# Performance work log

Measured on AMD Instinct MI355X. Metric: run time of the kernel, lower is better.

Reference implementation:

```python
import math
import jax, jax.numpy as jnp
import numpy as np

V, D, H, L, F, S, B = 32000, 768, 12, 6, 3072, 2048, 4
DK = D // H


def setup_inputs() -> dict:
    key = jax.random.key(0)
    ks = jax.random.split(key, 16)
    sc = 0.02
    n = jax.random.normal
    inp = {
        "input_ids": jax.random.randint(ks[0], (B, S), 0, V, dtype=jnp.int64)
        if jax.config.jax_enable_x64 else jax.random.randint(ks[0], (B, S), 0, V, dtype=jnp.int32),
        "emb": n(ks[1], (V, D), jnp.float32) * sc,
        "Wq": n(ks[2], (L, D, D), jnp.float32) * sc, "bq": jnp.zeros((L, D), jnp.float32),
        "Wk": n(ks[3], (L, D, D), jnp.float32) * sc, "bk": jnp.zeros((L, D), jnp.float32),
        "Wv": n(ks[4], (L, D, D), jnp.float32) * sc, "bv": jnp.zeros((L, D), jnp.float32),
        "Wo": n(ks[5], (L, D, D), jnp.float32) * sc, "bo": jnp.zeros((L, D), jnp.float32),
        "W1": n(ks[6], (L, D, F), jnp.float32) * sc, "b1": jnp.zeros((L, F), jnp.float32),
        "W2": n(ks[7], (L, F, D), jnp.float32) * sc, "b2": jnp.zeros((L, D), jnp.float32),
        "gamma": jnp.ones((L, D), jnp.float32), "beta": jnp.zeros((L, D), jnp.float32),
    }
    return inp


def _pos_encoding(seq_len, d):
    pos = jnp.arange(seq_len, dtype=jnp.float32)[:, None]                  # [S,1]
    div = jnp.exp(jnp.arange(0, d, 2, dtype=jnp.float32) * (-math.log(10000.0) / d))
    ang = pos * div                                                        # [S,D/2]
    return jnp.stack([jnp.sin(ang), jnp.cos(ang)], axis=-1).reshape(seq_len, d)


def _layernorm(x, g, b, eps=1e-5):
    mu = x.mean(-1, keepdims=True)
    var = ((x - mu) ** 2).mean(-1, keepdims=True)
    return (x - mu) * jax.lax.rsqrt(var + eps) * g + b


def _forward(input_ids, emb, Wq, bq, Wk, bk, Wv, bv, Wo, bo, W1, b1, W2, b2, gamma, beta):
    mask = (input_ids != 1)[:, None, None, :]                              # [B,1,1,S]
    x = emb[input_ids] + _pos_encoding(input_ids.shape[1], emb.shape[1])   # [B,S,D]

    def layer(x, p):
        wq, bq_, wk, bk_, wv, bv_, wo, bo_, w1, b1_, w2, b2_, g, bt = p
        def heads(h):  # [B,S,D] -> [B,H,S,DK]
            return h.reshape(B, S, H, DK).transpose(0, 2, 1, 3)
        q = heads(x @ wq + bq_)
        k = heads(x @ wk + bk_)
        v = heads(x @ wv + bv_)
        scores = jnp.einsum("bhqd,bhkd->bhqk", q, k) / math.sqrt(DK)
        scores = jnp.where(mask, scores, -1e9)
        attn = jax.nn.softmax(scores, axis=-1)
        o = jnp.einsum("bhqk,bhkd->bhqd", attn, v)
        o = o.transpose(0, 2, 1, 3).reshape(B, S, D) @ wo + bo_
        x1 = _layernorm(x + o, g, bt)
        ff = jax.nn.relu(x1 @ w1 + b1_) @ w2 + b2_
        return _layernorm(x1 + ff, g, bt), None  # same norm params reused (as in source)

    x, _ = jax.lax.scan(layer, x, (Wq, bq, Wk, bk, Wv, bv, Wo, bo, W1, b1, W2, b2, gamma, beta))
    return x.mean(axis=1)                                                  # [B,D]


def reference(input_ids, emb, Wq, bq, Wk, bk, Wv, bv, Wo, bo, W1, b1, W2, b2, gamma, beta):
    return _forward(input_ids, emb, Wq, bq, Wk, bk, Wv, bv, Wo, bo, W1, b1, W2, b2, gamma, beta)
```

## Files before the change

kernel.cpp:

```cpp
#include <hip/hip_runtime.h>
#include <hip/hip_bf16.h>
#include <math.h>

typedef unsigned short u16;
typedef unsigned long long u64;
using bf16x8 = __attribute__((ext_vector_type(8))) short;
using f32x4  = __attribute__((ext_vector_type(4))) float;

static constexpr int kD = 768;
static constexpr int kH = 12;
static constexpr int kL = 6;
static constexpr int kF = 3072;
static constexpr int kS = 2048;
static constexpr int kB = 4;
static constexpr int kQW = 2304;
static constexpr int kNT = kB * kS;

static constexpr float kQScale = 0.18033688011112043f;

__device__ __forceinline__ u16 f2bf(float f) {
    return __bfloat16_as_ushort(__float2bfloat16(f));
}
__device__ __forceinline__ float b2f(u16 u) {
    return __uint_as_float((unsigned)u << 16);
}
__device__ __forceinline__ unsigned cvtpk(float a, float b) {
    unsigned d;
    asm volatile("v_cvt_pk_bf16_f32 %0, %1, %2" : "=v"(d) : "v"(a), "v"(b));
    return d;
}
__device__ __forceinline__ float exp2fast(float x) {
#if __has_builtin(__builtin_amdgcn_exp2f)
    return __builtin_amdgcn_exp2f(x);
#else
    return __expf(x * 0.6931471805599453f);
#endif
}

__device__ __forceinline__ void gload16(const void* g, void* l) {
    auto gp = reinterpret_cast<const __attribute__((address_space(1))) unsigned int*>(
        reinterpret_cast<uintptr_t>(g));
    auto lp = reinterpret_cast<__attribute__((address_space(3))) unsigned int*>(
        reinterpret_cast<uintptr_t>(l));
    __builtin_amdgcn_global_load_lds(gp, lp, 16, 0, 0);
}

__global__ __launch_bounds__(256) void embed_pe(
    const int* __restrict__ ids, const float* __restrict__ emb,
    u16* __restrict__ xbf)
{
    const int t = blockIdx.x;
    const int s = t & (kS - 1);
    const int id = ids[t];
#pragma unroll
    for (int j = 0; j < 3; ++j) {
        const int d = threadIdx.x + (j << 8);
        const float i2 = (float)((d >> 1) << 1);
        const float dv = __expf(i2 * (-9.210340371976184f / 768.f));
        const float ang = (float)s * dv;
        const float pe = (d & 1) ? cosf(ang) : sinf(ang);
        xbf[(size_t)t * kD + d] = f2bf(emb[(size_t)id * kD + d] + pe);
    }
}

__global__ __launch_bounds__(256) void embed_pe_f32(
    const int* __restrict__ ids, const float* __restrict__ emb,
    float* __restrict__ x)
{
    const int t = blockIdx.x;
    const int s = t & (kS - 1);
    const int id = ids[t];
#pragma unroll
    for (int j = 0; j < 3; ++j) {
        const int d = threadIdx.x + (j << 8);
        const float i2 = (float)((d >> 1) << 1);
        const float dv = __expf(i2 * (-9.210340371976184f / 768.f));
        const float ang = (float)s * dv;
        const float pe = (d & 1) ? cosf(ang) : sinf(ang);
        x[(size_t)t * kD + d] = emb[(size_t)id * kD + d] + pe;
    }
}

__global__ __launch_bounds__(64) void mk_maskbits(const int* __restrict__ ids,
                                                  u64* __restrict__ mbits)
{
    const int w = blockIdx.x;
    const int lane = threadIdx.x;
    const u64 m = __ballot(ids[(size_t)w * 64 + lane] != 1);
    if (lane == 0) mbits[w] = m;
}

__global__ __launch_bounds__(256) void bias_build(
    const float* __restrict__ bq, const float* __restrict__ bk,
    const float* __restrict__ bv, const float* __restrict__ bo,
    const float* __restrict__ b1, const float* __restrict__ b2,
    float* __restrict__ ba)
{
    const int i = blockIdx.x * 256 + threadIdx.x;
    if (i >= 6 * 6912) return;
    const int l = i / 6912, p = i % 6912;
    float v;
    if      (p < 768)  v = bq[l * 768 + p] * kQScale;
    else if (p < 1536) v = bk[l * 768 + p - 768];
    else if (p < 2304) v = bv[l * 768 + p - 1536];
    else if (p < 3072) v = bo[l * 768 + p - 2304];
    else if (p < 6144) v = b1[(size_t)l * 3072 + p - 3072];
    else               v = b2[l * 768 + p - 6144];
    ba[i] = v;
}

static constexpr size_t OFF_WO = (size_t)2304 * 768;
static constexpr size_t OFF_W1 = OFF_WO + (size_t)768 * 768;
static constexpr size_t OFF_W2 = OFF_W1 + (size_t)3072 * 768;
static constexpr size_t WARENA_E = OFF_W2 + (size_t)768 * 3072;

__global__ __launch_bounds__(256) void cvt_all(
    const float* __restrict__ Wq, const float* __restrict__ Wk,
    const float* __restrict__ Wv, const float* __restrict__ Wo,
    const float* __restrict__ W1, const float* __restrict__ W2,
    u16* __restrict__ wa)
{
    __shared__ float T[64][68];
    const int t = blockIdx.x;
    const float* S; u16* Dp; int Nsrc, Kdst, srow0, scol0; float sc = 1.f;
    if (t < 432) {
        const int ni = t % 36, ki = t / 36;
        const int ng = ni * 64;
        const int sel = ng / 768;
        scol0 = ng % 768; srow0 = ki * 64;
        S = (sel == 0) ? Wq : (sel == 1) ? Wk : Wv;
        if (sel == 0) sc = kQScale;
        Nsrc = 768; Kdst = 768;
        Dp = wa + (size_t)ng * 768 + srow0;
    } else if (t < 576) {
        const int tt = t - 432; const int ni = tt % 12, ki = tt / 12;
        scol0 = ni * 64; srow0 = ki * 64;
        S = Wo; Nsrc = 768; Kdst = 768;
        Dp = wa + OFF_WO + (size_t)(ni * 64) * 768 + srow0;
    } else if (t < 1152) {
        const int tt = t - 576; const int ni = tt % 48, ki = tt / 48;
        scol0 = ni * 64; srow0 = ki * 64;
        S = W1; Nsrc = 3072; Kdst = 768;
        Dp = wa + OFF_W1 + (size_t)(ni * 64) * 768 + srow0;
    } else {
        const int tt = t - 1152; const int ni = tt % 12, ki = tt / 12;
        scol0 = ni * 64; srow0 = ki * 64;
        S = W2; Nsrc = 768; Kdst = 3072;
        Dp = wa + OFF_W2 + (size_t)(ni * 64) * 3072 + srow0;
    }
    const int tid = threadIdx.x;
#pragma unroll
    for (int i = 0; i < 4; ++i) {
        const int idx = tid + (i << 8);
        const int kr = idx >> 4;
        const int nc = (idx & 15) << 2;
        const float4 v = *(const float4*)(S + (size_t)(srow0 + kr) * Nsrc + scol0 + nc);
        T[kr][nc] = v.x; T[kr][nc + 1] = v.y; T[kr][nc + 2] = v.z; T[kr][nc + 3] = v.w;
    }
    __syncthreads();
#pragma unroll
    for (int i = 0; i < 4; ++i) {
        const int idx = tid + (i << 8);
        const int nr = idx >> 4;
        const int kc = (idx & 15) << 2;
        ushort4 o;
        o.x = f2bf(T[kc][nr] * sc);     o.y = f2bf(T[kc + 1][nr] * sc);
        o.z = f2bf(T[kc + 2][nr] * sc); o.w = f2bf(T[kc + 3][nr] * sc);
        *(ushort4*)(Dp + (size_t)nr * Kdst + kc) = o;
    }
}

__global__ __launch_bounds__(256, 2) void gemm256b(
    const u16* __restrict__ A, const u16* __restrict__ Bt,
    const float* __restrict__ bias, void* __restrict__ Cv,
    u16* __restrict__ vTp, int M, int N, int K, int mode)
{
    __shared__ u16 As[3][4096];
    __shared__ u16 Bs[3][8192];
    const int tid = threadIdx.x;
    const int l = tid & 63;
    const int lo = l & 15, hi = l >> 4;
    const int wc = tid >> 6;

    int brow = blockIdx.x, bcol = blockIdx.y;
    const int gx = gridDim.x;
    if ((gx & 7) == 0) {
        const int id = blockIdx.y * gx + blockIdx.x;
        const int xcd = id & 7, idx = id >> 3;
        const int rpx = gx >> 3;
        brow = xcd * rpx + (idx % rpx);
        bcol = idx / rpx;
    }
    const size_t row0 = (size_t)brow * 128;
    const size_t col0 = (size_t)bcol * 256;

    const int ca0 = tid, ca1 = tid + 256;
    const int ra0 = ca0 >> 2, ga0 = (ca0 & 3) ^ ((ra0 >> 1) & 3);
    const int ra1 = ca1 >> 2, ga1 = (ca1 & 3) ^ ((ra1 >> 1) & 3);
    const u16* aP0 = A + (row0 + ra0) * K + ga0 * 8;
    const u16* aP1 = A + (row0 + ra1) * K + ga1 * 8;
    const u16* bP[4];
#pragma unroll
    for (int q = 0; q < 4; ++q) {
        const int c = tid + (q << 8);
        const int r = c >> 2, g = (c & 3) ^ ((r >> 1) & 3);
        bP[q] = Bt + (col0 + r) * K + g * 8;
    }

    f32x4 acc[8][4];
#pragma unroll
    for (int i = 0; i < 8; ++i)
#pragma unroll
        for (int j = 0; j < 4; ++j)
#pragma unroll
            for (int r = 0; r < 4; ++r) acc[i][j][r] = 0.f;

    int aoff[8], boff[4];
#pragma unroll
    for (int i = 0; i < 8; ++i) {
        const int ra = i * 16 + lo;
        aoff[i] = ra * 32 + ((hi ^ ((ra >> 1) & 3)) << 3);
    }
#pragma unroll
    for (int j = 0; j < 4; ++j) {
        const int rb = wc * 64 + j * 16 + lo;
        boff[j] = rb * 32 + ((hi ^ ((rb >> 1) & 3)) << 3);
    }

    const int NT = K >> 5;
#pragma unroll
    for (int t = 0; t < 2; ++t) {
        const int k0 = t << 5;
        gload16(aP0 + k0, As[t] + ca0 * 8);
        gload16(aP1 + k0, As[t] + ca1 * 8);
#pragma unroll
        for (int q = 0; q < 4; ++q)
            gload16(bP[q] + k0, Bs[t] + (tid + (q << 8)) * 8);
    }

    int cur = 0;
    for (int t = 0; t < NT; ++t) {
        if (t + 1 < NT) {
            asm volatile("s_waitcnt vmcnt(6)" ::: "memory");
        } else {
            asm volatile("s_waitcnt vmcnt(0)" ::: "memory");
        }
        __builtin_amdgcn_s_barrier();
        if (t + 2 < NT) {
            const int k0 = (t + 2) << 5;
            const int nb = (cur + 2 >= 3) ? cur - 1 : cur + 2;
            gload16(aP0 + k0, As[nb] + ca0 * 8);
            gload16(aP1 + k0, As[nb] + ca1 * 8);
#pragma unroll
            for (int q = 0; q < 4; ++q)
                gload16(bP[q] + k0, Bs[nb] + (tid + (q << 8)) * 8);
        }
        bf16x8 af[8], bfr[4];
#pragma unroll
        for (int i = 0; i < 8; ++i) af[i]  = *(const bf16x8*)&As[cur][aoff[i]];
#pragma unroll
        for (int j = 0; j < 4; ++j) bfr[j] = *(const bf16x8*)&Bs[cur][boff[j]];
        __builtin_amdgcn_s_setprio(1);
#pragma unroll
        for (int i = 0; i < 8; ++i)
#pragma unroll
            for (int j = 0; j < 4; ++j)
                acc[i][j] = __builtin_amdgcn_mfma_f32_16x16x32_bf16(
                    af[i], bfr[j], acc[i][j], 0, 0, 0);
        __builtin_amdgcn_s_setprio(0);
        cur = (cur + 1 == 3) ? 0 : cur + 1;
    }

    const bool vmode = (mode == 3) && (col0 >= 1536);
    if (vmode) {
#pragma unroll
        for (int i = 0; i < 8; ++i) {
            const size_t rbase = row0 + i * 16 + hi * 4;
            const size_t tb = (rbase >> 6) * 64;
            const int k0 = (int)(rbase & 63);
            const int pos = (((k0 >> 2) & 3) << 3) + (((k0 >> 4) & 1) << 2)
                          + ((k0 >> 5) << 5);
#pragma unroll
            for (int j = 0; j < 4; ++j) {
                const size_t c = col0 + wc * 64 + j * 16 + lo;
                const float bs = bias[c];
                const size_t d = c - 1536;
                ushort4 o;
                o.x = f2bf(acc[i][j][0] + bs);
                o.y = f2bf(acc[i][j][1] + bs);
                o.z = f2bf(acc[i][j][2] + bs);
                o.w = f2bf(acc[i][j][3] + bs);
                *(ushort4*)(vTp + d * (size_t)M + tb + pos) = o;
            }
        }
        return;
    }

#pragma unroll
    for (int i = 0; i < 8; ++i) {
        const size_t rbase = row0 + i * 16 + hi * 4;
#pragma unroll
        for (int j = 0; j < 4; ++j) {
            const size_t c = col0 + wc * 64 + j * 16 + lo;
            const float bs = bias[c];
#pragma unroll
            for (int r = 0; r < 4; ++r) {
                float v = acc[i][j][r] + bs;
                if (mode == 2) v = fmaxf(v, 0.f);
                ((u16*)Cv)[(rbase + r) * (size_t)N + c] = f2bf(v);
            }
        }
    }
}

__global__ __launch_bounds__(256) void gemm_bf16(
    const u16* __restrict__ A, const u16* __restrict__ Bt,
    const float* __restrict__ bias, void* __restrict__ Cv,
    u16* __restrict__ vTp, int M, int N, int K, int mode)
{
    __shared__ u16 As[3][4096];
    __shared__ u16 Bs[3][4096];
    const int tid = threadIdx.x;
    const int l = tid & 63;
    const int lo = l & 15, hi = l >> 4;
    const int w = tid >> 6, wr = w >> 1, wc = w & 1;

    int brow = blockIdx.x, bcol = blockIdx.y;
    const int gx = gridDim.x;
    if ((gx & 7) == 0) {
        const int id = blockIdx.y * gx + blockIdx.x;
        const int xcd = id & 7, idx = id >> 3;
        const int rpx = gx >> 3;
        brow = xcd * rpx + (idx % rpx);
        bcol = idx / rpx;
    }
    const size_t row0 = (size_t)brow * 128;
    const size_t col0 = (size_t)bcol * 128;

    const int c0 = tid, c1 = tid + 256;
    const int r0 = c0 >> 2, g0 = (c0 & 3) ^ ((r0 >> 1) & 3);
    const int r1 = c1 >> 2, g1 = (c1 & 3) ^ ((r1 >> 1) & 3);
    const u16* a0 = A  + (row0 + r0) * K + g0 * 8;
    const u16* a1 = A  + (row0 + r1) * K + g1 * 8;
    const u16* b0 = Bt + (col0 + r0) * K + g0 * 8;
    const u16* b1 = Bt + (col0 + r1) * K + g1 * 8;

    f32x4 acc[4][4];
#pragma unroll
    for (int i = 0; i < 4; ++i)
#pragma unroll
        for (int j = 0; j < 4; ++j)
#pragma unroll
            for (int r = 0; r < 4; ++r) acc[i][j][r] = 0.f;

    int aoff[4], boff[4];
#pragma unroll
    for (int i = 0; i < 4; ++i) {
        const int ra = wr * 64 + i * 16 + lo;
        aoff[i] = ra * 32 + ((hi ^ ((ra >> 1) & 3)) << 3);
        const int rb = wc * 64 + i * 16 + lo;
        boff[i] = rb * 32 + ((hi ^ ((rb >> 1) & 3)) << 3);
    }

    const int NT = K >> 5;
#pragma unroll
    for (int t = 0; t < 2; ++t) {
        const int k0 = t << 5;
        gload16(a0 + k0, As[t] + c0 * 8);
        gload16(a1 + k0, As[t] + c1 * 8);
        gload16(b0 + k0, Bs[t] + c0 * 8);
        gload16(b1 + k0, Bs[t] + c1 * 8);
    }

    int cur = 0;
    for (int t = 0; t < NT; ++t) {
        if (t + 1 < NT) {
            asm volatile("s_waitcnt vmcnt(4)" ::: "memory");
        } else {
            asm volatile("s_waitcnt vmcnt(0)" ::: "memory");
        }
        __builtin_amdgcn_s_barrier();
        if (t + 2 < NT) {
            const int k0 = (t + 2) << 5;
            const int nb = (cur + 2 >= 3) ? cur - 1 : cur + 2;
            gload16(a0 + k0, As[nb] + c0 * 8);
            gload16(a1 + k0, As[nb] + c1 * 8);
            gload16(b0 + k0, Bs[nb] + c0 * 8);
            gload16(b1 + k0, Bs[nb] + c1 * 8);
        }
        bf16x8 af[4], bfr[4];
#pragma unroll
        for (int i = 0; i < 4; ++i) af[i]  = *(const bf16x8*)&As[cur][aoff[i]];
#pragma unroll
        for (int j = 0; j < 4; ++j) bfr[j] = *(const bf16x8*)&Bs[cur][boff[j]];
        __builtin_amdgcn_s_setprio(1);
#pragma unroll
        for (int i = 0; i < 4; ++i)
#pragma unroll
            for (int j = 0; j < 4; ++j)
                acc[i][j] = __builtin_amdgcn_mfma_f32_16x16x32_bf16(
                    af[i], bfr[j], acc[i][j], 0, 0, 0);
        __builtin_amdgcn_s_setprio(0);
        cur = (cur + 1 == 3) ? 0 : cur + 1;
    }

#pragma unroll
    for (int i = 0; i < 4; ++i) {
        const size_t rbase = row0 + wr * 64 + i * 16 + hi * 4;
#pragma unroll
        for (int j = 0; j < 4; ++j) {
            const size_t c = col0 + wc * 64 + j * 16 + lo;
            const float bs = bias[c];
#pragma unroll
            for (int r = 0; r < 4; ++r) {
                float v = acc[i][j][r] + bs;
                if (mode == 2) v = fmaxf(v, 0.f);
                ((u16*)Cv)[(rbase + r) * (size_t)N + c] = f2bf(v);
            }
        }
    }
}

__global__ __launch_bounds__(512) void attn_mfma(
    const u16* __restrict__ QKV, const u16* __restrict__ vT,
    const u64* __restrict__ mbits, u16* __restrict__ O)
{
    __shared__ u16 Ks[4][4096];
    __shared__ u16 Vs[4][4096];

    const int tid = threadIdx.x, l = tid & 63, w = tid >> 6;
    const int lo = l & 15, hi = l >> 4;

    const int flat = blockIdx.x + 16 * (blockIdx.y + 12 * blockIdx.z);
    const int nf = (flat & 7) * 96 + (flat >> 3);
    const int qi = nf & 15;
    const int h  = (nf >> 4) % 12;
    const int b  = nf / 192;
    const int q0 = qi << 7;

    bf16x8 qf0, qf1;
    {
        const u16* qp = QKV + ((size_t)(b * kS + q0 + w * 16 + lo)) * kQW
                            + h * 64 + hi * 8;
        qf0 = *(const bf16x8*)qp;
        qf1 = *(const bf16x8*)(qp + 32);
    }

    const int rw = tid >> 3, sx = tid & 7, E = sx ^ (rw & 7);
    const u16* Kbase = QKV + (size_t)(b * kS) * kQW + 768 + h * 64;
    const u16* Vbase = vT + (size_t)(h * 64) * kNT + b * kS;

    f32x4 accO[4];
#pragma unroll
    for (int n = 0; n < 4; ++n)
#pragma unroll
        for (int r = 0; r < 4; ++r) accO[n][r] = 0.f;
    float m = -3.0e38f, lsum = 0.f;

    const int ksw = (lo & 7) << 3;
    constexpr int NP = kS / 128;

#pragma unroll
    for (int t = 0; t < 2; ++t) {
        const size_t kof = (size_t)(t << 6) * kQW;
        const size_t vof = (size_t)(t << 6);
        gload16(Kbase + kof + (size_t)rw * kQW + E * 8, Ks[t] + tid * 8);
        gload16(Vbase + (size_t)rw * kNT + vof + E * 8, Vs[t] + tid * 8);
    }

    for (int it = 0; it < NP; ++it) {
        const int bA = (it & 1) << 1, bB = bA + 1;
        asm volatile("s_waitcnt vmcnt(0)" ::: "memory");
        __syncthreads();

        if (it + 1 < NP) {
            const int nA = ((it + 1) & 1) << 1, nB = nA + 1;
            const size_t kofA = (size_t)((2 * it + 2) << 6) * kQW;
            const size_t kofB = (size_t)((2 * it + 3) << 6) * kQW;
            const size_t vofA = (size_t)((2 * it + 2) << 6);
            const size_t vofB = (size_t)((2 * it + 3) << 6);
            gload16(Kbase + kofA + (size_t)rw * kQW + E * 8, Ks[nA] + tid * 8);
            gload16(Vbase + (size_t)rw * kNT + vofA + E * 8, Vs[nA] + tid * 8);
            gload16(Kbase + kofB + (size_t)rw * kQW + E * 8, Ks[nB] + tid * 8);
            gload16(Vbase + (size_t)rw * kNT + vofB + E * 8, Vs[nB] + tid * 8);
        }

        f32x4 stA[4], stB[4];
        __builtin_amdgcn_s_setprio(1);
#pragma unroll
        for (int j = 0; j < 4; ++j) {
#pragma unroll
            for (int r = 0; r < 4; ++r) { stA[j][r] = 0.f; stB[j][r] = 0.f; }
            const int kb2 = (j * 16 + lo) * 64;
            const bf16x8 a0 = *(const bf16x8*)&Ks[bA][kb2 + ((hi * 8)      ^ ksw)];
            const bf16x8 a1 = *(const bf16x8*)&Ks[bA][kb2 + ((hi * 8 + 32) ^ ksw)];
            const bf16x8 b0v = *(const bf16x8*)&Ks[bB][kb2 + ((hi * 8)      ^ ksw)];
            const bf16x8 b1v = *(const bf16x8*)&Ks[bB][kb2 + ((hi * 8 + 32) ^ ksw)];
            stA[j] = __builtin_amdgcn_mfma_f32_16x16x32_bf16(a0, qf0, stA[j], 0, 0, 0);
            stA[j] = __builtin_amdgcn_mfma_f32_16x16x32_bf16(a1, qf1, stA[j], 0, 0, 0);
            stB[j] = __builtin_amdgcn_mfma_f32_16x16x32_bf16(b0v, qf0, stB[j], 0, 0, 0);
            stB[j] = __builtin_amdgcn_mfma_f32_16x16x32_bf16(b1v, qf1, stB[j], 0, 0, 0);
        }
        __builtin_amdgcn_s_setprio(0);

        float rmax = stA[0][0];
#pragma unroll
        for (int j = 0; j < 4; ++j)
#pragma unroll
            for (int r = 0; r < 4; ++r) {
                rmax = fmaxf(rmax, stA[j][r]);
                rmax = fmaxf(rmax, stB[j][r]);
            }
        rmax = fmaxf(rmax, __shfl_xor(rmax, 16));
        rmax = fmaxf(rmax, __shfl_xor(rmax, 32));

        const bool skip = __all(rmax <= m + 11.0f);
        if (!skip) {
            const float mn = fmaxf(m, rmax);
            const float corr = exp2fast(m - mn);
            m = mn;
            lsum *= corr;
            float c2[4];
#pragma unroll
            for (int r = 0; r < 4; ++r) c2[r] = __shfl(corr, hi * 4 + r);
#pragma unroll
            for (int n = 0; n < 4; ++n)
#pragma unroll
                for (int r = 0; r < 4; ++r) accO[n][r] *= c2[r];
        }

#pragma unroll
        for (int j = 0; j < 4; ++j)
#pragma unroll
            for (int r = 0; r < 4; ++r) {
                stA[j][r] = exp2fast(stA[j][r] - m);
                stB[j][r] = exp2fast(stB[j][r] - m);
            }

        const u64 mbA = mbits[b * 32 + 2 * it];
        const u64 mbB = mbits[b * 32 + 2 * it + 1];
        if (mbA != ~0ull) {
#pragma unroll
            for (int j = 0; j < 4; ++j)
#pragma unroll
                for (int r = 0; r < 4; ++r)
                    if (!((mbA >> (j * 16 + hi * 4 + r)) & 1)) stA[j][r] = 0.f;
        }
        if (mbB != ~0ull) {
#pragma unroll
            for (int j = 0; j < 4; ++j)
#pragma unroll
                for (int r = 0; r < 4; ++r)
                    if (!((mbB >> (j * 16 + hi * 4 + r)) & 1)) stB[j][r] = 0.f;
        }

        float ts = 0.f;
#pragma unroll
        for (int j = 0; j < 4; ++j)
#pragma unroll
            for (int r = 0; r < 4; ++r) ts += stA[j][r] + stB[j][r];
        lsum += ts;

        union PU { unsigned u[4]; bf16x8 v; } p0, p1, p2, p3;
        p0.u[0] = cvtpk(stA[0][0], stA[0][1]); p0.u[1] = cvtpk(stA[0][2], stA[0][3]);
        p0.u[2] = cvtpk(stA[1][0], stA[1][1]); p0.u[3] = cvtpk(stA[1][2], stA[1][3]);
        p1.u[0] = cvtpk(stA[2][0], stA[2][1]); p1.u[1] = cvtpk(stA[2][2], stA[2][3]);
        p1.u[2] = cvtpk(stA[3][0], stA[3][1]); p1.u[3] = cvtpk(stA[3][2], stA[3][3]);
        p2.u[0] = cvtpk(stB[0][0], stB[0][1]); p2.u[1] = cvtpk(stB[0][2], stB[0][3]);
        p2.u[2] = cvtpk(stB[1][0], stB[1][1]); p2.u[3] = cvtpk(stB[1][2], stB[1][3]);
        p3.u[0] = cvtpk(stB[2][0], stB[2][1]); p3.u[1] = cvtpk(stB[2][2], stB[2][3]);
        p3.u[2] = cvtpk(stB[3][0], stB[3][1]); p3.u[3] = cvtpk(stB[3][2], stB[3][3]);

        __builtin_amdgcn_s_setprio(1);
#pragma unroll
        for (int n = 0; n < 4; ++n) {
            const int vb2 = (n * 16 + lo) * 64;
            const bf16x8 vA0 = *(const bf16x8*)&Vs[bA][vb2 + ((hi * 8)      ^ ksw)];
            const bf16x8 vA1 = *(const bf16x8*)&Vs[bA][vb2 + ((hi * 8 + 32) ^ ksw)];
            const bf16x8 vB0 = *(const bf16x8*)&Vs[bB][vb2 + ((hi * 8)      ^ ksw)];
            const bf16x8 vB1 = *(const bf16x8*)&Vs[bB][vb2 + ((hi * 8 + 32) ^ ksw)];
            accO[n] = __builtin_amdgcn_mfma_f32_16x16x32_bf16(p0.v, vA0, accO[n], 0, 0, 0);
            accO[n] = __builtin_amdgcn_mfma_f32_16x16x32_bf16(p1.v, vA1, accO[n], 0, 0, 0);
            accO[n] = __builtin_amdgcn_mfma_f32_16x16x32_bf16(p2.v, vB0, accO[n], 0, 0, 0);
            accO[n] = __builtin_amdgcn_mfma_f32_16x16x32_bf16(p3.v, vB1, accO[n], 0, 0, 0);
        }
        __builtin_amdgcn_s_setprio(0);
    }

    float ts = lsum;
    ts += __shfl_xor(ts, 16);
    ts += __shfl_xor(ts, 32);
    float linv[4];
#pragma unroll
    for (int r = 0; r < 4; ++r) linv[r] = 1.f / __shfl(ts, hi * 4 + r);
#pragma unroll
    for (int n = 0; n < 4; ++n)
#pragma unroll
        for (int r = 0; r < 4; ++r)
            O[((size_t)(b * kS + q0 + w * 16 + hi * 4 + r)) * kD
              + h * 64 + n * 16 + lo] = f2bf(accO[n][r] * linv[r]);
}

__global__ __launch_bounds__(256) void add_ln_bf(
    const u16* __restrict__ a, const u16* __restrict__ r,
    const float* __restrict__ g, const float* __restrict__ bt,
    u16* __restrict__ out)
{
    const int lane = threadIdx.x & 63;
    const size_t row = (size_t)blockIdx.x * 4 + (threadIdx.x >> 6);
    const ushort4* a4 = (const ushort4*)(a + row * kD);
    const ushort4* r4 = (const ushort4*)(r + row * kD);
    float v[3][4];
    float s = 0.f;
#pragma unroll
    for (int j = 0; j < 3; ++j) {
        const ushort4 av = a4[j * 64 + lane];
        const ushort4 rv = r4[j * 64 + lane];
        v[j][0] = b2f(av.x) + b2f(rv.x);
        v[j][1] = b2f(av.y) + b2f(rv.y);
        v[j][2] = b2f(av.z) + b2f(rv.z);
        v[j][3] = b2f(av.w) + b2f(rv.w);
        s += v[j][0] + v[j][1] + v[j][2] + v[j][3];
    }
#pragma unroll
    for (int off = 32; off; off >>= 1) s += __shfl_xor(s, off);
    const float mu = s * (1.f / 768.f);
    float vs = 0.f;
#pragma unroll
    for (int j = 0; j < 3; ++j)
#pragma unroll
        for (int e = 0; e < 4; ++e) {
            const float t0 = v[j][e] - mu;
            vs = fmaf(t0, t0, vs);
        }
#pragma unroll
    for (int off = 32; off; off >>= 1) vs += __shfl_xor(vs, off);
    const float rstd = rsqrtf(vs * (1.f / 768.f) + 1e-5f);
    const float4* g4 = (const float4*)g;
    const float4* b4 = (const float4*)bt;
#pragma unroll
    for (int j = 0; j < 3; ++j) {
        const float4 gv = g4[j * 64 + lane];
        const float4 bv = b4[j * 64 + lane];
        ushort4 o;
        o.x = f2bf((v[j][0] - mu) * rstd * gv.x + bv.x);
        o.y = f2bf((v[j][1] - mu) * rstd * gv.y + bv.y);
        o.z = f2bf((v[j][2] - mu) * rstd * gv.z + bv.z);
        o.w = f2bf((v[j][3] - mu) * rstd * gv.w + bv.w);
        ((ushort4*)(out + row * kD))[j * 64 + lane] = o;
    }
}

__global__ __launch_bounds__(192) void mean_part_bf(
    const u16* __restrict__ x, float* __restrict__ mred)
{
    const int c = blockIdx.x, b = blockIdx.y;
    const int d = threadIdx.x * 4;
    const u16* base = x + ((size_t)b * kS + c * 32) * kD + d;
    float s0 = 0.f, s1 = 0.f, s2 = 0.f, s3 = 0.f;
#pragma unroll 8
    for (int t = 0; t < 32; ++t) {
        const ushort4 u = *(const ushort4*)(base + (size_t)t * kD);
        s0 += b2f(u.x); s1 += b2f(u.y); s2 += b2f(u.z); s3 += b2f(u.w);
    }
    float4 o; o.x = s0; o.y = s1; o.z = s2; o.w = s3;
    *(float4*)(mred + ((size_t)b * 64 + c) * kD + d) = o;
}

__global__ __launch_bounds__(256) void mean_fin(
    const float* __restrict__ mred, float* __restrict__ out)
{
    const int d = blockIdx.x * 256 + threadIdx.x;
    const int b = blockIdx.y;
    float s = 0.f;
#pragma unroll
    for (int c = 0; c < 64; ++c) s += mred[((size_t)b * 64 + c) * kD + d];
    out[b * kD + d] = s * (1.f / 2048.f);
}

__global__ __launch_bounds__(256) void add_ln_f32(
    const float* __restrict__ a, const float* __restrict__ r,
    const float* __restrict__ g, const float* __restrict__ bt,
    float* __restrict__ out)
{
    const int lane = threadIdx.x & 63;
    const size_t row = (size_t)blockIdx.x * 4 + (threadIdx.x >> 6);
    const float4* a4 = (const float4*)(a + row * kD);
    const float4* r4 = (const float4*)(r + row * kD);
    float4 v[3];
    float s = 0.f;
#pragma unroll
    for (int j = 0; j < 3; ++j) {
        const float4 av = a4[j * 64 + lane];
        const float4 rv = r4[j * 64 + lane];
        v[j].x = av.x + rv.x; v[j].y = av.y + rv.y;
        v[j].z = av.z + rv.z; v[j].w = av.w + rv.w;
        s += v[j].x + v[j].y + v[j].z + v[j].w;
    }
#pragma unroll
    for (int off = 32; off; off >>= 1) s += __shfl_xor(s, off);
    const float mu = s * (1.f / 768.f);
    float vs = 0.f;
#pragma unroll
    for (int j = 0; j < 3; ++j) {
        float t0 = v[j].x - mu, t1 = v[j].y - mu, t2 = v[j].z - mu, t3 = v[j].w - mu;
        vs = fmaf(t0, t0, fmaf(t1, t1, fmaf(t2, t2, fmaf(t3, t3, vs))));
    }
#pragma unroll
    for (int off = 32; off; off >>= 1) vs += __shfl_xor(vs, off);
    const float rstd = rsqrtf(vs * (1.f / 768.f) + 1e-5f);
    const float4* g4 = (const float4*)g;
    const float4* b4 = (const float4*)bt;
#pragma unroll
    for (int j = 0; j < 3; ++j) {
        const float4 gv = g4[j * 64 + lane];
        const float4 bv = b4[j * 64 + lane];
        float4 o;
        o.x = (v[j].x - mu) * rstd * gv.x + bv.x;
        o.y = (v[j].y - mu) * rstd * gv.y + bv.y;
        o.z = (v[j].z - mu) * rstd * gv.z + bv.z;
        o.w = (v[j].w - mu) * rstd * gv.w + bv.w;
        ((float4*)(out + row * kD))[j * 64 + lane] = o;
    }
}

__global__ __launch_bounds__(256) void mean_s(
    const float* __restrict__ x, float* __restrict__ out)
{
    const int d = blockIdx.x * 256 + threadIdx.x;
    const int b = blockIdx.y;
    float s = 0.f;
    for (int t = 0; t < kS; ++t) s += x[((size_t)b * kS + t) * kD + d];
    out[b * kD + d] = s * (1.f / 2048.f);
}

__global__ __launch_bounds__(256) void gemm_f32(
    const float* __restrict__ A, const float* __restrict__ W,
    const float* __restrict__ bias, float* __restrict__ C,
    int M, int N, int K, int relu)
{
    __shared__ float As[16][68];
    __shared__ float Bs[16][68];
    const int tid = threadIdx.x;
    const int row0 = blockIdx.x << 6;
    const int col0 = blockIdx.y << 6;
    const int tx = tid & 15, ty = tid >> 4;
    const int ar = tid >> 2;
    const int ak = (tid & 3) << 2;
    const int bk = tid >> 4;
    const int bc = (tid & 15) << 2;
    float acc[4][4] = {};
    const float* Ap = A + (size_t)(row0 + ar) * K + ak;
    const float* Wp = W + (size_t)bk * N + col0 + bc;
    for (int k0 = 0; k0 < K; k0 += 16) {
        const float4 a4 = *(const float4*)(Ap + k0);
        const float4 b4 = *(const float4*)(Wp + (size_t)k0 * N);
        __syncthreads();
        As[ak + 0][ar] = a4.x; As[ak + 1][ar] = a4.y;
        As[ak + 2][ar] = a4.z; As[ak + 3][ar] = a4.w;
        *(float4*)&Bs[bk][bc] = b4;
        __syncthreads();
#pragma unroll
        for (int kk = 0; kk < 16; ++kk) {
            const float4 av = *(const float4*)&As[kk][ty << 2];
            const float4 bv = *(const float4*)&Bs[kk][tx << 2];
            const float aa[4] = {av.x, av.y, av.z, av.w};
            const float bb[4] = {bv.x, bv.y, bv.z, bv.w};
#pragma unroll
            for (int i = 0; i < 4; ++i)
#pragma unroll
                for (int j = 0; j < 4; ++j)
                    acc[i][j] = fmaf(aa[i], bb[j], acc[i][j]);
        }
    }
#pragma unroll
    for (int i = 0; i < 4; ++i) {
        const int row = row0 + (ty << 2) + i;
#pragma unroll
        for (int j = 0; j < 4; ++j) {
            const int col = col0 + (tx << 2) + j;
            float v = acc[i][j] + bias[col];
            if (relu) v = fmaxf(v, 0.f);
            C[(size_t)row * N + col] = v;
        }
    }
}

__global__ __launch_bounds__(256) void attn_fused(
    const float* __restrict__ Q, const float* __restrict__ Km,
    const float* __restrict__ Vm, const int* __restrict__ ids,
    float* __restrict__ O)
{
    __shared__ float Ksf[64 * 64];
    __shared__ float Vtf[64 * 64];
    __shared__ float Qs[16][64];
    __shared__ float Psf[4][4][64];
    const int tid = threadIdx.x;
    const int w = tid >> 6;
    const int lane = tid & 63;
    const int h = blockIdx.y, b = blockIdx.z;
    const int qrow0 = blockIdx.x << 4;
    {
        const int r = tid >> 4;
        const int c4 = tid & 15;
        const float4 q4 = *(const float4*)(
            Q + ((size_t)(b * kS + qrow0 + r)) * kD + h * 64 + (c4 << 2));
        Qs[r][(c4 << 2) + 0] = q4.x * 0.125f;
        Qs[r][(c4 << 2) + 1] = q4.y * 0.125f;
        Qs[r][(c4 << 2) + 2] = q4.z * 0.125f;
        Qs[r][(c4 << 2) + 3] = q4.w * 0.125f;
    }
    float m[4], lsum[4], o[4];
#pragma unroll
    for (int r = 0; r < 4; ++r) { m[r] = -3.0e38f; lsum[r] = 0.f; o[r] = 0.f; }
    for (int kt = 0; kt < kS / 64; ++kt) {
        __syncthreads();
#pragma unroll
        for (int i = 0; i < 4; ++i) {
            const int lin = tid + (i << 8);
            const int row = lin >> 4;
            const int s4 = lin & 15;
            const size_t gro = ((size_t)(b * kS + (kt << 6) + row)) * kD + h * 64 + (s4 << 2);
            const float4 k4 = *(const float4*)(Km + gro);
            ((float4*)Ksf)[(row << 4) + (s4 ^ (row & 7))] = k4;
            const float4 v4 = *(const float4*)(Vm + gro);
            const int ksl = row >> 2, ke = row & 3;
            const int d0 = s4 << 2;
            Vtf[(d0 + 0) * 64 + ((ksl ^ ((d0 + 0) & 7)) << 2) + ke] = v4.x;
            Vtf[(d0 + 1) * 64 + ((ksl ^ ((d0 + 1) & 7)) << 2) + ke] = v4.y;
            Vtf[(d0 + 2) * 64 + ((ksl ^ ((d0 + 2) & 7)) << 2) + ke] = v4.z;
            Vtf[(d0 + 3) * 64 + ((ksl ^ ((d0 + 3) & 7)) << 2) + ke] = v4.w;
        }
        __syncthreads();
        const bool masked = (ids[(size_t)b * kS + (kt << 6) + lane] == 1);
        float scr[4] = {0.f, 0.f, 0.f, 0.f};
#pragma unroll
        for (int i16 = 0; i16 < 16; ++i16) {
            const float4 kv = ((const float4*)Ksf)[(lane << 4) + (i16 ^ (lane & 7))];
#pragma unroll
            for (int r = 0; r < 4; ++r) {
                const float4 qv = *(const float4*)&Qs[(w << 2) + r][i16 << 2];
                scr[r] = fmaf(kv.x, qv.x, fmaf(kv.y, qv.y,
                          fmaf(kv.z, qv.z, fmaf(kv.w, qv.w, scr[r]))));
            }
        }
#pragma unroll
        for (int r = 0; r < 4; ++r) {
            float sm = masked ? -3.0e38f : scr[r];
#pragma unroll
            for (int off = 32; off; off >>= 1) sm = fmaxf(sm, __shfl_xor(sm, off));
            const float mn = fmaxf(m[r], sm);
            const float cr = __expf(m[r] - mn);
            const float pv = masked ? 0.f : __expf(scr[r] - mn);
            float ps = pv;
#pragma unroll
            for (int off = 32; off; off >>= 1) ps += __shfl_xor(ps, off);
            lsum[r] = lsum[r] * cr + ps;
            o[r] *= cr;
            m[r] = mn;
            Psf[w][r][lane] = pv;
        }
#pragma unroll
        for (int i16 = 0; i16 < 16; ++i16) {
            const float4 vv = ((const float4*)Vtf)[(lane << 4) + (i16 ^ (lane & 7))];
#pragma unroll
            for (int r = 0; r < 4; ++r) {
                const float4 pv = *(const float4*)&Psf[w][r][i16 << 2];
                o[r] = fmaf(pv.x, vv.x, fmaf(pv.y, vv.y,
                        fmaf(pv.z, vv.z, fmaf(pv.w, vv.w, o[r]))));
            }
        }
    }
#pragma unroll
    for (int r = 0; r < 4; ++r)
        O[((size_t)(b * kS + qrow0 + (w << 2) + r)) * kD + h * 64 + lane] =
            o[r] / lsum[r];
}

extern "C" void kernel_launch(void* const* d_in, const int* in_sizes, int n_in,
                              void* d_out, int out_size, void* d_ws, size_t ws_size,
                              hipStream_t stream)
{
    const int*   ids   = (const int*)  d_in[0];
    const float* emb   = (const float*)d_in[1];
    const float* Wq    = (const float*)d_in[2];
    const float* bq    = (const float*)d_in[3];
    const float* Wk    = (const float*)d_in[4];
    const float* bk    = (const float*)d_in[5];
    const float* Wv    = (const float*)d_in[6];
    const float* bv    = (const float*)d_in[7];
    const float* Wo    = (const float*)d_in[8];
    const float* bo    = (const float*)d_in[9];
    const float* W1    = (const float*)d_in[10];
    const float* b1    = (const float*)d_in[11];
    const float* W2    = (const float*)d_in[12];
    const float* b2    = (const float*)d_in[13];
    const float* gamma = (const float*)d_in[14];
    const float* beta  = (const float*)d_in[15];
    float* out = (float*)d_out;

    const size_t BUFE = (size_t)kB * kS * kD;
    const size_t WDD  = (size_t)kD * kD;
    const size_t WDF  = (size_t)kD * kF;
    const size_t HIDE = (size_t)kB * kS * kF;
    const int NTOK = kB * kS;

    const size_t NEED = BUFE * 2 * 4
                      + HIDE * 2
                      + WARENA_E * 2
                      + (size_t)6 * 6912 * 4
                      + 128 * 8
                      + (size_t)kB * 64 * kD * 4;

    if (ws_size >= NEED) {
        u16*   xb  = (u16*)d_ws;
        u16*   x1b = xb + BUFE;
        u16*   ao  = x1b + BUFE;
        u16*   ob  = ao + BUFE;
        u16*   sc  = ob + BUFE;
        u16*   vtb = sc + (size_t)NTOK * kQW;
        u16*   wa  = sc + HIDE;
        float* ba  = (float*)(wa + WARENA_E);
        u64*   mbt = (u64*)(ba + 6 * 6912);
        float* mrd = (float*)(mbt + 128);

        embed_pe<<<NTOK, 256, 0, stream>>>(ids, emb, xb);
        mk_maskbits<<<kB * kS / 64, 64, 0, stream>>>(ids, mbt);
        bias_build<<<(6 * 6912 + 255) / 256, 256, 0, stream>>>(
            bq, bk, bv, bo, b1, b2, ba);

        for (int l = 0; l < kL; ++l) {
            const size_t oDD = (size_t)l * WDD;
            const size_t oDF = (size_t)l * WDF;
            const float* bl = ba + (size_t)l * 6912;
            const float* gl  = gamma + (size_t)l * kD;
            const float* btl = beta  + (size_t)l * kD;

            cvt_all<<<1728, 256, 0, stream>>>(
                Wq + oDD, Wk + oDD, Wv + oDD, Wo + oDD, W1 + oDF, W2 + oDF, wa);

            gemm256b<<<dim3(64, 9), 256, 0, stream>>>(
                xb, wa, bl, sc, vtb, NTOK, kQW, kD, 3);

            attn_mfma<<<dim3(kS / 128, kH, kB), 512, 0, stream>>>(
                sc, vtb, mbt, ao);

            gemm_bf16<<<dim3(64, 6), 256, 0, stream>>>(
                ao, wa + OFF_WO, bl + 2304, ob, nullptr, NTOK, kD, kD, 1);

            add_ln_bf<<<NTOK / 4, 256, 0, stream>>>(xb, ob, gl, btl, x1b);

            gemm256b<<<dim3(64, 12), 256, 0, stream>>>(
                x1b, wa + OFF_W1, bl + 3072, sc, nullptr, NTOK, kF, kD, 2);
            gemm_bf16<<<dim3(64, 6), 256, 0, stream>>>(
                sc, wa + OFF_W2, bl + 6144, ob, nullptr, NTOK, kD, kF, 1);

            add_ln_bf<<<NTOK / 4, 256, 0, stream>>>(x1b, ob, gl, btl, xb);
        }

        mean_part_bf<<<dim3(64, kB), 192, 0, stream>>>(xb, mrd);
        mean_fin<<<dim3(kD / 256, kB), 256, 0, stream>>>(mrd, out);
        return;
    }

    if (ws_size < 5 * BUFE * sizeof(float)) return;
    float* xb = (float*)d_ws;
    float* kb = xb + BUFE;
    float* qb = kb + BUFE;
    float* vb = qb + BUFE;
    float* obf = vb + BUFE;
    float* hb = qb;

    embed_pe_f32<<<NTOK, 256, 0, stream>>>(ids, emb, xb);
    for (int l = 0; l < kL; ++l) {
        const size_t oDD = (size_t)l * WDD;
        const size_t oDF = (size_t)l * WDF;
        gemm_f32<<<dim3(NTOK / 64, kD / 64), 256, 0, stream>>>(
            xb, Wq + oDD, bq + (size_t)l * kD, qb, NTOK, kD, kD, 0);
        gemm_f32<<<dim3(NTOK / 64, kD / 64), 256, 0, stream>>>(
            xb, Wk + oDD, bk + (size_t)l * kD, kb, NTOK, kD, kD, 0);
        gemm_f32<<<dim3(NTOK / 64, kD / 64), 256, 0, stream>>>(
            xb, Wv + oDD, bv + (size_t)l * kD, vb, NTOK, kD, kD, 0);
        attn_fused<<<dim3(kS / 16, kH, kB), 256, 0, stream>>>(qb, kb, vb, ids, obf);
        gemm_f32<<<dim3(NTOK / 64, kD / 64), 256, 0, stream>>>(
            obf, Wo + oDD, bo + (size_t)l * kD, qb, NTOK, kD, kD, 0);
        add_ln_f32<<<NTOK / 4, 256, 0, stream>>>(xb, qb,
            gamma + (size_t)l * kD, beta + (size_t)l * kD, kb);
        for (int c = 0; c < 2; ++c) {
            const size_t ro = (size_t)c * 4096;
            gemm_f32<<<dim3(4096 / 64, kF / 64), 256, 0, stream>>>(
                kb + ro * kD, W1 + oDF, b1 + (size_t)l * kF, hb, 4096, kF, kD, 1);
            gemm_f32<<<dim3(4096 / 64, kD / 64), 256, 0, stream>>>(
                hb, W2 + oDF, b2 + (size_t)l * kD, obf + ro * kD, 4096, kD, kF, 0);
        }
        add_ln_f32<<<NTOK / 4, 256, 0, stream>>>(kb, obf,
            gamma + (size_t)l * kD, beta + (size_t)l * kD, xb);
    }
    mean_s<<<dim3(kD / 256, kB), 256, 0, stream>>>(xb, out);
}
```

Baseline: 1.485 ms.

## Process two 16-row query groups per wave in attention to reuse K/V LDS reads

```diff
diff --git a/kernel.cpp b/kernel.cpp
--- a/kernel.cpp
+++ b/kernel.cpp
@@ -421,7 +421,7 @@
     }
 }
 
-__global__ __launch_bounds__(512) void attn_mfma(
+__global__ __launch_bounds__(256) void attn_mfma(
     const u16* __restrict__ QKV, const u16* __restrict__ vT,
     const u64* __restrict__ mbits, u16* __restrict__ O)
 {
@@ -438,24 +438,30 @@
     const int b  = nf / 192;
     const int q0 = qi << 7;
 
-    bf16x8 qf0, qf1;
-    {
-        const u16* qp = QKV + ((size_t)(b * kS + q0 + w * 16 + lo)) * kQW
+    bf16x8 qf[2][2];
+#pragma unroll
+    for (int g = 0; g < 2; ++g) {
+        const u16* qp = QKV + ((size_t)(b * kS + q0 + w * 32 + g * 16 + lo)) * kQW
                             + h * 64 + hi * 8;
-        qf0 = *(const bf16x8*)qp;
-        qf1 = *(const bf16x8*)(qp + 32);
-    }
-
-    const int rw = tid >> 3, sx = tid & 7, E = sx ^ (rw & 7);
+        qf[g][0] = *(const bf16x8*)qp;
+        qf[g][1] = *(const bf16x8*)(qp + 32);
+    }
+
+    const int gA = tid, gB = tid + 256;
+    const int rwA = gA >> 3, sxA = gA & 7, EA = sxA ^ (rwA & 7);
+    const int rwB = gB >> 3, sxB = gB & 7, EB = sxB ^ (rwB & 7);
     const u16* Kbase = QKV + (size_t)(b * kS) * kQW + 768 + h * 64;
     const u16* Vbase = vT + (size_t)(h * 64) * kNT + b * kS;
 
-    f32x4 accO[4];
-#pragma unroll
-    for (int n = 0; n < 4; ++n)
-#pragma unroll
-        for (int r = 0; r < 4; ++r) accO[n][r] = 0.f;
-    float m = -3.0e38f, lsum = 0.f;
+    f32x4 accO[2][4];
+#pragma unroll
+    for (int g = 0; g < 2; ++g)
+#pragma unroll
+        for (int n = 0; n < 4; ++n)
+#pragma unroll
+            for (int r = 0; r < 4; ++r) accO[g][n][r] = 0.f;
+    float m[2] = {-3.0e38f, -3.0e38f};
+    float lsum[2] = {0.f, 0.f};
 
     const int ksw = (lo & 7) << 3;
     constexpr int NP = kS / 128;
@@ -464,8 +470,10 @@
     for (int t = 0; t < 2; ++t) {
         const size_t kof = (size_t)(t << 6) * kQW;
         const size_t vof = (size_t)(t << 6);
-        gload16(Kbase + kof + (size_t)rw * kQW + E * 8, Ks[t] + tid * 8);
-        gload16(Vbase + (size_t)rw * kNT + vof + E * 8, Vs[t] + tid * 8);
+        gload16(Kbase + kof + (size_t)rwA * kQW + EA * 8, Ks[t] + gA * 8);
+        gload16(Kbase + kof + (size_t)rwB * kQW + EB * 8, Ks[t] + gB * 8);
+        gload16(Vbase + (size_t)rwA * kNT + vof + EA * 8, Vs[t] + gA * 8);
+        gload16(Vbase + (size_t)rwB * kNT + vof + EB * 8, Vs[t] + gB * 8);
     }
 
     for (int it = 0; it < NP; ++it) {
@@ -479,126 +487,142 @@
             const size_t kofB = (size_t)((2 * it + 3) << 6) * kQW;
             const size_t vofA = (size_t)((2 * it + 2) << 6);
             const size_t vofB = (size_t)((2 * it + 3) << 6);
-            gload16(Kbase + kofA + (size_t)rw * kQW + E * 8, Ks[nA] + tid * 8);
-            gload16(Vbase + (size_t)rw * kNT + vofA + E * 8, Vs[nA] + tid * 8);
-            gload16(Kbase + kofB + (size_t)rw * kQW + E * 8, Ks[nB] + tid * 8);
-            gload16(Vbase + (size_t)rw * kNT + vofB + E * 8, Vs[nB] + tid * 8);
-        }
-
-        f32x4 stA[4], stB[4];
+            gload16(Kbase + kofA + (size_t)rwA * kQW + EA * 8, Ks[nA] + gA * 8);
+            gload16(Kbase + kofA + (size_t)rwB * kQW + EB * 8, Ks[nA] + gB * 8);
+            gload16(Vbase + (size_t)rwA * kNT + vofA + EA * 8, Vs[nA] + gA * 8);
+            gload16(Vbase + (size_t)rwB * kNT + vofA + EB * 8, Vs[nA] + gB * 8);
+            gload16(Kbase + kofB + (size_t)rwA * kQW + EA * 8, Ks[nB] + gA * 8);
+            gload16(Kbase + kofB + (size_t)rwB * kQW + EB * 8, Ks[nB] + gB * 8);
+            gload16(Vbase + (size_t)rwA * kNT + vofB + EA * 8, Vs[nB] + gA * 8);
+            gload16(Vbase + (size_t)rwB * kNT + vofB + EB * 8, Vs[nB] + gB * 8);
+        }
+
+        f32x4 stA[2][4], stB[2][4];
         __builtin_amdgcn_s_setprio(1);
 #pragma unroll
         for (int j = 0; j < 4; ++j) {
-#pragma unroll
-            for (int r = 0; r < 4; ++r) { stA[j][r] = 0.f; stB[j][r] = 0.f; }
             const int kb2 = (j * 16 + lo) * 64;
             const bf16x8 a0 = *(const bf16x8*)&Ks[bA][kb2 + ((hi * 8)      ^ ksw)];
             const bf16x8 a1 = *(const bf16x8*)&Ks[bA][kb2 + ((hi * 8 + 32) ^ ksw)];
             const bf16x8 b0v = *(const bf16x8*)&Ks[bB][kb2 + ((hi * 8)      ^ ksw)];
             const bf16x8 b1v = *(const bf16x8*)&Ks[bB][kb2 + ((hi * 8 + 32) ^ ksw)];
-            stA[j] = __builtin_amdgcn_mfma_f32_16x16x32_bf16(a0, qf0, stA[j], 0, 0, 0);
-            stA[j] = __builtin_amdgcn_mfma_f32_16x16x32_bf16(a1, qf1, stA[j], 0, 0, 0);
-            stB[j] = __builtin_amdgcn_mfma_f32_16x16x32_bf16(b0v, qf0, stB[j], 0, 0, 0);
-            stB[j] = __builtin_amdgcn_mfma_f32_16x16x32_bf16(b1v, qf1, stB[j], 0, 0, 0);
+#pragma unroll
+            for (int g = 0; g < 2; ++g) {
+#pragma unroll
+                for (int r = 0; r < 4; ++r) { stA[g][j][r] = 0.f; stB[g][j][r] = 0.f; }
+                stA[g][j] = __builtin_amdgcn_mfma_f32_16x16x32_bf16(a0, qf[g][0], stA[g][j], 0, 0, 0);
+                stA[g][j] = __builtin_amdgcn_mfma_f32_16x16x32_bf16(a1, qf[g][1], stA[g][j], 0, 0, 0);
+                stB[g][j] = __builtin_amdgcn_mfma_f32_16x16x32_bf16(b0v, qf[g][0], stB[g][j], 0, 0, 0);
+                stB[g][j] = __builtin_amdgcn_mfma_f32_16x16x32_bf16(b1v, qf[g][1], stB[g][j], 0, 0, 0);
+            }
         }
         __builtin_amdgcn_s_setprio(0);
-
-        float rmax = stA[0][0];
-#pragma unroll
-        for (int j = 0; j < 4; ++j)
-#pragma unroll
-            for (int r = 0; r < 4; ++r) {
-                rmax = fmaxf(rmax, stA[j][r]);
-                rmax = fmaxf(rmax, stB[j][r]);
-            }
-        rmax = fmaxf(rmax, __shfl_xor(rmax, 16));
-        rmax = fmaxf(rmax, __shfl_xor(rmax, 32));
-
-        const bool skip = __all(rmax <= m + 11.0f);
-        if (!skip) {
-            const float mn = fmaxf(m, rmax);
-            const float corr = exp2fast(m - mn);
-            m = mn;
-            lsum *= corr;
-            float c2[4];
-#pragma unroll
-            for (int r = 0; r < 4; ++r) c2[r] = __shfl(corr, hi * 4 + r);
-#pragma unroll
-            for (int n = 0; n < 4; ++n)
-#pragma unroll
-                for (int r = 0; r < 4; ++r) accO[n][r] *= c2[r];
-        }
-
-#pragma unroll
-        for (int j = 0; j < 4; ++j)
-#pragma unroll
-            for (int r = 0; r < 4; ++r) {
-                stA[j][r] = exp2fast(stA[j][r] - m);
-                stB[j][r] = exp2fast(stB[j][r] - m);
-            }
 
         const u64 mbA = mbits[b * 32 + 2 * it];
         const u64 mbB = mbits[b * 32 + 2 * it + 1];
-        if (mbA != ~0ull) {
+
+#pragma unroll
+        for (int g = 0; g < 2; ++g) {
+            float rmax = stA[g][0][0];
 #pragma unroll
             for (int j = 0; j < 4; ++j)
 #pragma unroll
-                for (int r = 0; r < 4; ++r)
-                    if (!((mbA >> (j * 16 + hi * 4 + r)) & 1)) stA[j][r] = 0.f;
-        }
-        if (mbB != ~0ull) {
+                for (int r = 0; r < 4; ++r) {
+                    rmax = fmaxf(rmax, stA[g][j][r]);
+                    rmax = fmaxf(rmax, stB[g][j][r]);
+                }
+            rmax = fmaxf(rmax, __shfl_xor(rmax, 16));
+            rmax = fmaxf(rmax, __shfl_xor(rmax, 32));
+
+            const bool skip = __all(rmax <= m[g] + 11.0f);
+            if (!skip) {
+                const float mn = fmaxf(m[g], rmax);
+                const float corr = exp2fast(m[g] - mn);
+                m[g] = mn;
+                lsum[g] *= corr;
+                float c2[4];
+#pragma unroll
+                for (int r = 0; r < 4; ++r) c2[r] = __shfl(corr, hi * 4 + r);
+#pragma unroll
+                for (int n = 0; n < 4; ++n)
+#pragma unroll
+                    for (int r = 0; r < 4; ++r) accO[g][n][r] *= c2[r];
+            }
+
 #pragma unroll
             for (int j = 0; j < 4; ++j)
 #pragma unroll
-                for (int r = 0; r < 4; ++r)
-                    if (!((mbB >> (j * 16 + hi * 4 + r)) & 1)) stB[j][r] = 0.f;
-        }
-
-        float ts = 0.f;
-#pragma unroll
-        for (int j = 0; j < 4; ++j)
-#pragma unroll
-            for (int r = 0; r < 4; ++r) ts += stA[j][r] + stB[j][r];
-        lsum += ts;
-
-        union PU { unsigned u[4]; bf16x8 v; } p0, p1, p2, p3;
-        p0.u[0] = cvtpk(stA[0][0], stA[0][1]); p0.u[1] = cvtpk(stA[0][2], stA[0][3]);
-        p0.u[2] = cvtpk(stA[1][0], stA[1][1]); p0.u[3] = cvtpk(stA[1][2], stA[1][3]);
-        p1.u[0] = cvtpk(stA[2][0], stA[2][1]); p1.u[1] = cvtpk(stA[2][2], stA[2][3]);
-        p1.u[2] = cvtpk(stA[3][0], stA[3][1]); p1.u[3] = cvtpk(stA[3][2], stA[3][3]);
-        p2.u[0] = cvtpk(stB[0][0], stB[0][1]); p2.u[1] = cvtpk(stB[0][2], stB[0][3]);
-        p2.u[2] = cvtpk(stB[1][0], stB[1][1]); p2.u[3] = cvtpk(stB[1][2], stB[1][3]);
-        p3.u[0] = cvtpk(stB[2][0], stB[2][1]); p3.u[1] = cvtpk(stB[2][2], stB[2][3]);
-        p3.u[2] = cvtpk(stB[3][0], stB[3][1]); p3.u[3] = cvtpk(stB[3][2], stB[3][3]);
+                for (int r = 0; r < 4; ++r) {
+                    stA[g][j][r] = exp2fast(stA[g][j][r] - m[g]);
+                    stB[g][j][r] = exp2fast(stB[g][j][r] - m[g]);
+                }
+
+            if (mbA != ~0ull) {
+#pragma unroll
+                for (int j = 0; j < 4; ++j)
+#pragma unroll
+                    for (int r = 0; r < 4; ++r)
+                        if (!((mbA >> (j * 16 + hi * 4 + r)) & 1)) stA[g][j][r] = 0.f;
+            }
+            if (mbB != ~0ull) {
+#pragma unroll
+                for (int j = 0; j < 4; ++j)
+#pragma unroll
+                    for (int r = 0; r < 4; ++r)
+                        if (!((mbB >> (j * 16 + hi * 4 + r)) & 1)) stB[g][j][r] = 0.f;
+            }
+
+            float ts = 0.f;
+#pragma unroll
+            for (int j = 0; j < 4; ++j)
+#pragma unroll
+                for (int r = 0; r < 4; ++r) ts += stA[g][j][r] + stB[g][j][r];
+            lsum[g] += ts;
+        }
 
         __builtin_amdgcn_s_setprio(1);
 #pragma unroll
-        for (int n = 0; n < 4; ++n) {
-            const int vb2 = (n * 16 + lo) * 64;
-            const bf16x8 vA0 = *(const bf16x8*)&Vs[bA][vb2 + ((hi * 8)      ^ ksw)];
-            const bf16x8 vA1 = *(const bf16x8*)&Vs[bA][vb2 + ((hi * 8 + 32) ^ ksw)];
-            const bf16x8 vB0 = *(const bf16x8*)&Vs[bB][vb2 + ((hi * 8)      ^ ksw)];
-            const bf16x8 vB1 = *(const bf16x8*)&Vs[bB][vb2 + ((hi * 8 + 32) ^ ksw)];
-            accO[n] = __builtin_amdgcn_mfma_f32_16x16x32_bf16(p0.v, vA0, accO[n], 0, 0, 0);
-            accO[n] = __builtin_amdgcn_mfma_f32_16x16x32_bf16(p1.v, vA1, accO[n], 0, 0, 0);
-            accO[n] = __builtin_amdgcn_mfma_f32_16x16x32_bf16(p2.v, vB0, accO[n], 0, 0, 0);
-            accO[n] = __builtin_amdgcn_mfma_f32_16x16x32_bf16(p3.v, vB1, accO[n], 0, 0, 0);
+        for (int g = 0; g < 2; ++g) {
+            union PU { unsigned u[4]; bf16x8 v; } p0, p1, p2, p3;
+            p0.u[0] = cvtpk(stA[g][0][0], stA[g][0][1]); p0.u[1] = cvtpk(stA[g][0][2], stA[g][0][3]);
+            p0.u[2] = cvtpk(stA[g][1][0], stA[g][1][1]); p0.u[3] = cvtpk(stA[g][1][2], stA[g][1][3]);
+            p1.u[0] = cvtpk(stA[g][2][0], stA[g][2][1]); p1.u[1] = cvtpk(stA[g][2][2], stA[g][2][3]);
+            p1.u[2] = cvtpk(stA[g][3][0], stA[g][3][1]); p1.u[3] = cvtpk(stA[g][3][2], stA[g][3][3]);
+            p2.u[0] = cvtpk(stB[g][0][0], stB[g][0][1]); p2.u[1] = cvtpk(stB[g][0][2], stB[g][0][3]);
+            p2.u[2] = cvtpk(stB[g][1][0], stB[g][1][1]); p2.u[3] = cvtpk(stB[g][1][2], stB[g][1][3]);
+            p3.u[0] = cvtpk(stB[g][2][0], stB[g][2][1]); p3.u[1] = cvtpk(stB[g][2][2], stB[g][2][3]);
+            p3.u[2] = cvtpk(stB[g][3][0], stB[g][3][1]); p3.u[3] = cvtpk(stB[g][3][2], stB[g][3][3]);
+#pragma unroll
+            for (int n = 0; n < 4; ++n) {
+                const int vb2 = (n * 16 + lo) * 64;
+                const bf16x8 vA0 = *(const bf16x8*)&Vs[bA][vb2 + ((hi * 8)      ^ ksw)];
+                const bf16x8 vA1 = *(const bf16x8*)&Vs[bA][vb2 + ((hi * 8 + 32) ^ ksw)];
+                const bf16x8 vB0 = *(const bf16x8*)&Vs[bB][vb2 + ((hi * 8)      ^ ksw)];
+                const bf16x8 vB1 = *(const bf16x8*)&Vs[bB][vb2 + ((hi * 8 + 32) ^ ksw)];
+                accO[g][n] = __builtin_amdgcn_mfma_f32_16x16x32_bf16(p0.v, vA0, accO[g][n], 0, 0, 0);
+                accO[g][n] = __builtin_amdgcn_mfma_f32_16x16x32_bf16(p1.v, vA1, accO[g][n], 0, 0, 0);
+                accO[g][n] = __builtin_amdgcn_mfma_f32_16x16x32_bf16(p2.v, vB0, accO[g][n], 0, 0, 0);
+                accO[g][n] = __builtin_amdgcn_mfma_f32_16x16x32_bf16(p3.v, vB1, accO[g][n], 0, 0, 0);
+            }
         }
         __builtin_amdgcn_s_setprio(0);
     }
 
-    float ts = lsum;
-    ts += __shfl_xor(ts, 16);
-    ts += __shfl_xor(ts, 32);
-    float linv[4];
-#pragma unroll
-    for (int r = 0; r < 4; ++r) linv[r] = 1.f / __shfl(ts, hi * 4 + r);
-#pragma unroll
-    for (int n = 0; n < 4; ++n)
-#pragma unroll
-        for (int r = 0; r < 4; ++r)
-            O[((size_t)(b * kS + q0 + w * 16 + hi * 4 + r)) * kD
-              + h * 64 + n * 16 + lo] = f2bf(accO[n][r] * linv[r]);
+#pragma unroll
+    for (int g = 0; g < 2; ++g) {
+        float ts = lsum[g];
+        ts += __shfl_xor(ts, 16);
+        ts += __shfl_xor(ts, 32);
+        float linv[4];
+#pragma unroll
+        for (int r = 0; r < 4; ++r) linv[r] = 1.f / __shfl(ts, hi * 4 + r);
+#pragma unroll
+        for (int n = 0; n < 4; ++n)
+#pragma unroll
+            for (int r = 0; r < 4; ++r)
+                O[((size_t)(b * kS + q0 + w * 32 + g * 16 + hi * 4 + r)) * kD
+                  + h * 64 + n * 16 + lo] = f2bf(accO[g][n][r] * linv[r]);
+    }
 }
 
 __global__ __launch_bounds__(256) void add_ln_bf(
@@ -942,7 +966,7 @@
             gemm256b<<<dim3(64, 9), 256, 0, stream>>>(
                 xb, wa, bl, sc, vtb, NTOK, kQW, kD, 3);
 
-            attn_mfma<<<dim3(kS / 128, kH, kB), 512, 0, stream>>>(
+            attn_mfma<<<dim3(kS / 128, kH, kB), 256, 0, stream>>>(
                 sc, vtb, mbt, ao);
 
             gemm_bf16<<<dim3(64, 6), 256, 0, stream>>>(
```

Measured after the change: 1.717 ms. 1.16x slower.
